# Optimization experiments

Hardware: AMD Instinct MI355X
Metric: run time of the kernel (lower is better)

Reference implementation:

```python
import jax, jax.numpy as jnp
import numpy as np

M, IN, OUT = 8192, 4096, 4096
XOR_MASK = (1 << 3) | (1 << 7)  # 0x88: flips sign bit of each packed nibble


def _dequant_int4(weight_packed, weight_scales):
    """Decode packed int4 weights (offset-binary nibbles) to scaled float.

    weight_packed: [OUT, IN//2] int32, each byte holds two nibbles (v+8).
    Low nibble -> even input column, high nibble -> odd input column.
    """
    w = jnp.bitwise_xor(weight_packed, XOR_MASK)  # offset-binary -> two's complement nibbles
    low = jnp.bitwise_and(w, 0xF)
    high = jnp.bitwise_and(jnp.right_shift(w, 4), 0xF)
    low = jnp.where(low >= 8, low - 16, low)    # signed int4 in [-8, 7]
    high = jnp.where(high >= 8, high - 16, high)
    # interleave nibbles: [OUT, IN//2, 2] -> [OUT, IN]
    deq = jnp.stack([low, high], axis=-1).reshape(weight_packed.shape[0], -1)
    return deq.astype(weight_scales.dtype) * weight_scales[:, None]  # [OUT, IN]


def setup_inputs() -> dict:
    key = jax.random.key(0)
    k1, k2, k3, k4 = jax.random.split(key, 4)
    x = jax.random.normal(k1, (M, IN), dtype=jnp.float32)
    weight_packed = jax.random.randint(k2, (OUT, IN // 2), 0, 256, dtype=jnp.int32)
    weight_scales = jax.random.uniform(k3, (OUT,), dtype=jnp.float32) * 0.02 + 1e-3
    bias = jax.random.normal(k4, (OUT,), dtype=jnp.float32)
    return {"x": x, "weight_packed": weight_packed,
            "weight_scales": weight_scales, "bias": bias}


def reference(x, weight_packed, weight_scales, bias):
    # w4a16 forward: dequantize int4 weights per output row, then GEMM + bias.
    w = _dequant_int4(weight_packed, weight_scales)  # [OUT, IN]
    return jnp.dot(x, w.T) + bias  # [M, OUT]
```

## Files before the change

kernel.cpp:

```cpp
#include <hip/hip_runtime.h>
#include <cstdint>
#include <cstddef>

#define M_DIM 8192
#define K_DIM 4096
#define N_DIM 4096

#define BM 256
#define BN 256
#define BK 64
#define NT (K_DIM / BK)

typedef unsigned short u16;
typedef __bf16 bf16x8 __attribute__((ext_vector_type(8)));
typedef u16 u16x8 __attribute__((ext_vector_type(8)));
typedef float f32x4 __attribute__((ext_vector_type(4)));

__device__ __forceinline__ u16 f2bf_rne(float f) {
  uint32_t u = __builtin_bit_cast(uint32_t, f);
  return (u16)((u + 0x7FFFu + ((u >> 16) & 1u)) >> 16);
}
__device__ __forceinline__ u16 i2bf(int i) {
  return (u16)(__builtin_bit_cast(uint32_t, (float)i) >> 16);
}

#define XBLKS 16384
#define WBLKS 8192

__global__ __launch_bounds__(256) void prep(const float* __restrict__ x,
                                            const int* __restrict__ wp,
                                            u16* __restrict__ xb,
                                            u16* __restrict__ wb) {
  const int b = blockIdx.x;
  if (b < XBLKS) {
    size_t t = (size_t)b * 256 + threadIdx.x;
    const float4* xp = (const float4*)x;
    float4 a = xp[2 * t];
    float4 c = xp[2 * t + 1];
    u16x8 r;
    r[0] = f2bf_rne(a.x); r[1] = f2bf_rne(a.y); r[2] = f2bf_rne(a.z); r[3] = f2bf_rne(a.w);
    r[4] = f2bf_rne(c.x); r[5] = f2bf_rne(c.y); r[6] = f2bf_rne(c.z); r[7] = f2bf_rne(c.w);
    ((u16x8*)xb)[t] = r;
  } else {
    size_t t = (size_t)(b - XBLKS) * 256 + threadIdx.x;
    int4 p = ((const int4*)wp)[t];
    u16x8 r;
    int v;
    v = p.x ^ 0x88; r[0] = i2bf((v << 28) >> 28); r[1] = i2bf((v << 24) >> 28);
    v = p.y ^ 0x88; r[2] = i2bf((v << 28) >> 28); r[3] = i2bf((v << 24) >> 28);
    v = p.z ^ 0x88; r[4] = i2bf((v << 28) >> 28); r[5] = i2bf((v << 24) >> 28);
    v = p.w ^ 0x88; r[6] = i2bf((v << 28) >> 28); r[7] = i2bf((v << 24) >> 28);
    ((u16x8*)wb)[t] = r;
  }
}

__global__ __launch_bounds__(512, 2) void gemm_bt_w4a16(
    const u16* __restrict__ A,
    const u16* __restrict__ B,
    const float* __restrict__ scales,
    const float* __restrict__ bias,
    float* __restrict__ C) {
  __shared__ u16 sA0[3][128 * 64];
  __shared__ u16 sA1[2][128 * 64];
  __shared__ u16 sB0[2][128 * 64];
  __shared__ u16 sB1[2][128 * 64];

  const int tid = threadIdx.x;
  const int lane = tid & 63;
  const int wave = tid >> 6;
  const int m0 = blockIdx.y * BM;
  const int n0 = blockIdx.x * BN;

  const int wm = (wave >> 2) * 128;
  const int wn = (wave & 3) * 64;
  const int lrow = lane & 15;
  const int quad = lane >> 4;
  const int brw0 = wn & 64;

  f32x4 acc[8][4] = {};

  const int srow = tid >> 3;
  const int schunk = ((tid & 7) ^ (srow & 7)) * 8;
  const u16* ga = A + (size_t)(m0 + srow) * K_DIM + schunk;
  const u16* gb = B + (size_t)(n0 + srow) * K_DIM + schunk;
  const int dst0 = tid * 16;

#define GLDS(gp, lp)                                                      \
  __builtin_amdgcn_global_load_lds(                                       \
      (const __attribute__((address_space(1))) void*)(gp),                \
      (__attribute__((address_space(3))) void*)(lp), 16, 0, 0)

  auto stA0 = [&](int slot, int T) {
    const u16* g = ga + (size_t)T * BK;
    char* d = (char*)sA0[slot] + dst0;
    GLDS(g, d);
    GLDS(g + (size_t)64 * K_DIM, d + 8192);
  };
  auto stA1 = [&](int b, int T) {
    const u16* g = ga + (size_t)128 * K_DIM + (size_t)T * BK;
    char* d = (char*)sA1[b] + dst0;
    GLDS(g, d);
    GLDS(g + (size_t)64 * K_DIM, d + 8192);
  };
  auto stB0 = [&](int b, int T) {
    const u16* g = gb + (size_t)T * BK;
    char* d = (char*)sB0[b] + dst0;
    GLDS(g, d);
    GLDS(g + (size_t)64 * K_DIM, d + 8192);
  };
  auto stB1 = [&](int b, int T) {
    const u16* g = gb + (size_t)128 * K_DIM + (size_t)T * BK;
    char* d = (char*)sB1[b] + dst0;
    GLDS(g, d);
    GLDS(g + (size_t)64 * K_DIM, d + 8192);
  };

  stA0(0, 0); stA1(0, 0); stB0(0, 0); stB1(0, 0);

  int a0slot = 0;
#pragma unroll 1
  for (int T = 0; T < NT; ++T) {
    const int buf = T & 1;
    const int nbuf = buf ^ 1;
    const bool more = (T + 1 < NT);
    int a0next = a0slot + 1; if (a0next == 3) a0next = 0;

    if (more) {
      stA0(a0next, T + 1);
      asm volatile("s_waitcnt vmcnt(2)" ::: "memory");
    } else {
      asm volatile("s_waitcnt vmcnt(0)" ::: "memory");
    }
    __builtin_amdgcn_s_barrier();
    __builtin_amdgcn_sched_barrier(0);

    const u16* aH = (wave < 4) ? sA0[a0slot] : sA1[buf];
    const u16* bH = (wn < 128) ? sB0[buf] : sB1[buf];

#pragma unroll
    for (int s = 0; s < 2; ++s) {
      const int kc = ((s * 4 + quad) ^ (lrow & 7)) * 8;
      u16x8 bfr[4];
#pragma unroll
      for (int j = 0; j < 4; ++j)
        bfr[j] = *(const u16x8*)(bH + (brw0 + j * 16 + lrow) * BK + kc);
#pragma unroll
      for (int ih = 0; ih < 2; ++ih) {
        u16x8 af[4];
#pragma unroll
        for (int i = 0; i < 4; ++i)
          af[i] = *(const u16x8*)(aH + (ih * 64 + i * 16 + lrow) * BK + kc);
        if (more) {
          if (s == 0 && ih == 0) stA1(nbuf, T + 1);
          if (s == 0 && ih == 1) stB0(nbuf, T + 1);
          if (s == 1 && ih == 0) stB1(nbuf, T + 1);
        }
        __builtin_amdgcn_s_setprio(1);
#pragma unroll
        for (int i = 0; i < 4; ++i)
#pragma unroll
          for (int j = 0; j < 4; ++j)
            acc[ih * 4 + i][j] = __builtin_amdgcn_mfma_f32_16x16x32_bf16(
                __builtin_bit_cast(bf16x8, af[i]),
                __builtin_bit_cast(bf16x8, bfr[j]), acc[ih * 4 + i][j], 0, 0, 0);
        __builtin_amdgcn_s_setprio(0);
        __builtin_amdgcn_sched_barrier(0);
      }
    }
    a0slot = a0next;
  }

#pragma unroll
  for (int j = 0; j < 4; ++j) {
    const int n = n0 + wn + j * 16 + lrow;
    const float sc = scales[n];
    const float bi = bias[n];
#pragma unroll
    for (int i = 0; i < 8; ++i) {
      const int m = m0 + wm + i * 16 + quad * 4;
      float* cp = &C[(size_t)m * N_DIM + n];
#pragma unroll
      for (int r = 0; r < 4; ++r)
        cp[(size_t)r * N_DIM] = acc[i][j][r] * sc + bi;
    }
  }
#undef GLDS
}

__global__ __launch_bounds__(256) void fallback_w4a16(
    const float* __restrict__ x, const int* __restrict__ wp,
    const float* __restrict__ scales, const float* __restrict__ bias,
    float* __restrict__ out) {
  const int n = blockIdx.x * 256 + threadIdx.x;
  const int m = blockIdx.y;
  const float* xr = x + (size_t)m * K_DIM;
  const int* wr = wp + (size_t)n * (K_DIM / 2);
  float acc = 0.f;
  for (int j = 0; j < K_DIM / 2; ++j) {
    int w = wr[j] ^ 0x88;
    float lo = (float)((w << 28) >> 28);
    float hi = (float)((w << 24) >> 28);
    acc += xr[2 * j] * lo + xr[2 * j + 1] * hi;
  }
  out[(size_t)m * N_DIM + n] = acc * scales[n] + bias[n];
}

extern "C" void kernel_launch(void* const* d_in, const int* in_sizes, int n_in,
                              void* d_out, int out_size, void* d_ws, size_t ws_size,
                              hipStream_t stream) {
  const float* x = (const float*)d_in[0];
  const int* wp = (const int*)d_in[1];
  const float* sc = (const float*)d_in[2];
  const float* bi = (const float*)d_in[3];
  float* out = (float*)d_out;

  const size_t xb_elems = (size_t)M_DIM * K_DIM;
  const size_t wb_elems = (size_t)N_DIM * K_DIM;
  const size_t need = (xb_elems + wb_elems) * sizeof(u16);

  if (ws_size >= need) {
    u16* xb = (u16*)d_ws;
    u16* wb = xb + xb_elems;
    prep<<<XBLKS + WBLKS, 256, 0, stream>>>(x, wp, xb, wb);
    gemm_bt_w4a16<<<dim3(N_DIM / BN, M_DIM / BM), 512, 0, stream>>>(xb, wb, sc, bi, out);
  } else {
    fallback_w4a16<<<dim3(N_DIM / 256, M_DIM), 256, 0, stream>>>(x, wp, sc, bi, out);
  }
}
```

Measured before the change: 469.7 us.

## Switch GEMM inner loop to 32x32x16 bf16 MFMA with software-pipelined fragment loads

Replaces the 16x16x32 MFMA tiling (8x4 tiles per wave) with 32x32x16 MFMA (4x2 tiles per wave). The inner loop is restructured into four k-step clusters, and each step's LDS fragments are loaded ahead of the previous cluster's MFMAs. Larger MFMA tiles cut LDS fragment reads per flop and improve the issue ratio. The prefetched fragments raise register pressure. The epilogue is remapped to the 32x32 accumulator layout.

```diff
diff --git a/kernel.cpp b/kernel.cpp
--- a/kernel.cpp
+++ b/kernel.cpp
@@ -14,7 +14,7 @@
 typedef unsigned short u16;
 typedef __bf16 bf16x8 __attribute__((ext_vector_type(8)));
 typedef u16 u16x8 __attribute__((ext_vector_type(8)));
-typedef float f32x4 __attribute__((ext_vector_type(4)));
+typedef float f32x16 __attribute__((ext_vector_type(16)));
 
 __device__ __forceinline__ u16 f2bf_rne(float f) {
   uint32_t u = __builtin_bit_cast(uint32_t, f);
@@ -73,11 +73,13 @@
 
   const int wm = (wave >> 2) * 128;
   const int wn = (wave & 3) * 64;
-  const int lrow = lane & 15;
-  const int quad = lane >> 4;
   const int brw0 = wn & 64;
 
-  f32x4 acc[8][4] = {};
+  const int arow = lane & 31;
+  const int kq = lane >> 5;
+  const int key = lane & 7;
+
+  f32x16 acc[4][2] = {};
 
   const int srow = tid >> 3;
   const int schunk = ((tid & 7) ^ (srow & 7)) * 8;
@@ -114,6 +116,9 @@
     GLDS(g, d);
     GLDS(g + (size_t)64 * K_DIM, d + 8192);
   };
+
+  struct fragA { u16x8 v[4]; };
+  struct fragB { u16x8 v[2]; };
 
   stA0(0, 0); stA1(0, 0); stB0(0, 0); stB1(0, 0);
 
@@ -137,51 +142,67 @@
     const u16* aH = (wave < 4) ? sA0[a0slot] : sA1[buf];
     const u16* bH = (wn < 128) ? sB0[buf] : sB1[buf];
 
-#pragma unroll
-    for (int s = 0; s < 2; ++s) {
-      const int kc = ((s * 4 + quad) ^ (lrow & 7)) * 8;
-      u16x8 bfr[4];
-#pragma unroll
-      for (int j = 0; j < 4; ++j)
-        bfr[j] = *(const u16x8*)(bH + (brw0 + j * 16 + lrow) * BK + kc);
-#pragma unroll
-      for (int ih = 0; ih < 2; ++ih) {
-        u16x8 af[4];
-#pragma unroll
-        for (int i = 0; i < 4; ++i)
-          af[i] = *(const u16x8*)(aH + (ih * 64 + i * 16 + lrow) * BK + kc);
-        if (more) {
-          if (s == 0 && ih == 0) stA1(nbuf, T + 1);
-          if (s == 0 && ih == 1) stB0(nbuf, T + 1);
-          if (s == 1 && ih == 0) stB1(nbuf, T + 1);
-        }
-        __builtin_amdgcn_s_setprio(1);
-#pragma unroll
-        for (int i = 0; i < 4; ++i)
-#pragma unroll
-          for (int j = 0; j < 4; ++j)
-            acc[ih * 4 + i][j] = __builtin_amdgcn_mfma_f32_16x16x32_bf16(
-                __builtin_bit_cast(bf16x8, af[i]),
-                __builtin_bit_cast(bf16x8, bfr[j]), acc[ih * 4 + i][j], 0, 0, 0);
-        __builtin_amdgcn_s_setprio(0);
-        __builtin_amdgcn_sched_barrier(0);
-      }
-    }
+    auto ldA = [&](int ks) {
+      fragA f;
+      const int sl = ((ks * 2 + kq) ^ key) * 8;
+#pragma unroll
+      for (int t = 0; t < 4; ++t)
+        f.v[t] = *(const u16x8*)(aH + (t * 32 + arow) * BK + sl);
+      return f;
+    };
+    auto ldB = [&](int ks) {
+      fragB f;
+      const int sl = ((ks * 2 + kq) ^ key) * 8;
+#pragma unroll
+      for (int t = 0; t < 2; ++t)
+        f.v[t] = *(const u16x8*)(bH + (brw0 + t * 32 + arow) * BK + sl);
+      return f;
+    };
+
+#define CLUSTER(fa, fb)                                                   \
+  __builtin_amdgcn_s_setprio(1);                                          \
+  _Pragma("unroll")                                                       \
+  for (int tm = 0; tm < 4; ++tm)                                          \
+    _Pragma("unroll")                                                     \
+    for (int tn = 0; tn < 2; ++tn)                                        \
+      acc[tm][tn] = __builtin_amdgcn_mfma_f32_32x32x16_bf16(              \
+          __builtin_bit_cast(bf16x8, fa.v[tm]),                           \
+          __builtin_bit_cast(bf16x8, fb.v[tn]), acc[tm][tn], 0, 0, 0);    \
+  __builtin_amdgcn_s_setprio(0);
+
+    fragA fa0 = ldA(0); fragB fb0 = ldB(0);
+    fragA fa1 = ldA(1); fragB fb1 = ldB(1);
+    if (more) stA1(nbuf, T + 1);
+    CLUSTER(fa0, fb0);
+
+    fragA fa2 = ldA(2); fragB fb2 = ldB(2);
+    if (more) stB0(nbuf, T + 1);
+    CLUSTER(fa1, fb1);
+
+    fragA fa3 = ldA(3); fragB fb3 = ldB(3);
+    if (more) stB1(nbuf, T + 1);
+    CLUSTER(fa2, fb2);
+
+    CLUSTER(fa3, fb3);
+#undef CLUSTER
+
+    __builtin_amdgcn_sched_barrier(0);
     a0slot = a0next;
   }
 
 #pragma unroll
-  for (int j = 0; j < 4; ++j) {
-    const int n = n0 + wn + j * 16 + lrow;
+  for (int tn = 0; tn < 2; ++tn) {
+    const int n = n0 + wn + tn * 32 + arow;
     const float sc = scales[n];
     const float bi = bias[n];
 #pragma unroll
-    for (int i = 0; i < 8; ++i) {
-      const int m = m0 + wm + i * 16 + quad * 4;
-      float* cp = &C[(size_t)m * N_DIM + n];
-#pragma unroll
-      for (int r = 0; r < 4; ++r)
-        cp[(size_t)r * N_DIM] = acc[i][j][r] * sc + bi;
+    for (int tm = 0; tm < 4; ++tm) {
+      const int mb = m0 + wm + tm * 32 + 4 * kq;
+#pragma unroll
+      for (int r = 0; r < 16; ++r) {
+        const int m = mb + (r & 3) + 8 * (r >> 2);
+        C[(size_t)m * N_DIM + n] = acc[tm][tn][r] * sc + bi;
+      }
     }
   }
 #undef GLDS
```

Measured after the change: 493.2 us. 5.0% more time.
